# Kernel tuning notes

Measured on AMD Instinct MI355X. Metric: run time of the kernel, lower is better.

## Reference

```python
import jax, jax.numpy as jnp
import numpy as np

B, T, CIN = 8, 4096, 512
GROUP, ENTRY = 2, 320
COUT = 512
D = COUT // GROUP  # per-group codebook dim = 256


def setup_inputs() -> dict:
    key = jax.random.key(0)
    k_x, k_w, k_cb, k_g = jax.random.split(key, 4)
    x = jax.random.normal(k_x, (B, T, CIN), dtype=jnp.float32)
    # weight_proj: Linear(in_channel, group*entry)
    Wp = jax.random.normal(k_w, (GROUP * ENTRY, CIN), dtype=jnp.float32) * (1.0 / np.sqrt(CIN))
    bp = jnp.zeros((GROUP * ENTRY,), dtype=jnp.float32)
    # stacked codebooks: [group, entry, out_channel//group]
    codebooks = jax.random.normal(k_cb, (GROUP, ENTRY, D), dtype=jnp.float32)
    # pre-sampled gumbel noise (torch gumbel_softmax samples this internally)
    gumbel = jax.random.gumbel(k_g, (B, T, GROUP * ENTRY), dtype=jnp.float32)
    return {"x": x, "Wp": Wp, "bp": bp, "codebooks": codebooks, "gumbel": gumbel}


def reference(x, Wp, bp, codebooks, gumbel):
    # weight_proj
    logits = jnp.einsum('btc,ec->bte', x, Wp) + bp          # [B,T,group*entry]
    # gumbel_softmax(tau=1, hard=False, dim=-1): softmax over full group*entry axis
    y = jax.nn.softmax(logits + gumbel, axis=-1)            # [B,T,group*entry]
    # chunk into groups -> contiguous reshape matches torch.chunk
    yg = y.reshape(B, T, GROUP, ENTRY)                      # [B,T,G,E]
    # per-group matmul against codebook weights, then concat over groups
    out = jnp.einsum('btge,ged->btgd', yg, codebooks)       # [B,T,G,D]
    return out.reshape(B, T, GROUP * D)                     # [B,T,out_channel]
```

## Files before the change

kernel.cpp:

```cpp
#include <hip/hip_runtime.h>
#include <hip/hip_bf16.h>
#include <stdint.h>

#define BT     32768
#define CIN    512
#define NE     640
#define ENTRY  320
#define DD     256
#define MROWS  32
#define TPB    256

using bf16x8 = __attribute__((ext_vector_type(8))) short;
using f32x4  = __attribute__((ext_vector_type(4))) float;

#define A_OFF   0
#define A_STR   80
#define B_OFF   2560
#define Y_OFF   0
#define Y_STR   648
#define S_OFF   41472
#define CB_OFF  41600
#define SMEM_BYTES 74368

__device__ __forceinline__ unsigned short f2b(float f) {
    union { float f; uint32_t u; } v; v.f = f;
    uint32_t u = v.u;
    return (unsigned short)((u + 0x7FFFu + ((u >> 16) & 1u)) >> 16);
}

__device__ __forceinline__ void gl2lds16(const void* g, void* l) {
    __builtin_amdgcn_global_load_lds((const __attribute__((address_space(1))) void*)g,
                                     (__attribute__((address_space(3))) void*)l, 16, 0, 0);
}

__global__ void prep_kernel(const float* __restrict__ Wp, const float* __restrict__ cb,
                            unsigned short* __restrict__ WpB, unsigned short* __restrict__ cbT) {
    int i = blockIdx.x * blockDim.x + threadIdx.x;
    if (i < NE * CIN) {
        WpB[i] = f2b(Wp[i]);
    } else {
        int o = i - NE * CIN;
        if (o < 2 * ENTRY * DD) {
            int g = o / (DD * ENTRY);
            int r = o - g * (DD * ENTRY);
            int d = r / ENTRY;
            int e = r - d * ENTRY;
            cbT[o] = f2b(cb[(g * ENTRY + e) * DD + d]);
        }
    }
}

__global__ __launch_bounds__(TPB, 2) void fused_kernel(
    const float* __restrict__ x, const float* __restrict__ bp,
    const float* __restrict__ gum, const unsigned short* __restrict__ WpB,
    const unsigned short* __restrict__ cbT, float* __restrict__ out) {

    extern __shared__ char smem[];
    unsigned short* yS = (unsigned short*)(smem + Y_OFF);
    float*          sS = (float*)(smem + S_OFF);
    char*           aS = smem + A_OFF;
    char*           bS = smem + B_OFF;
    char*           cS = smem + CB_OFF;

    const int tid = threadIdx.x;
    const int w  = tid >> 6;
    const int l  = tid & 63;
    const int q  = l >> 4;
    const int ln = l & 15;
    const int rowbase = blockIdx.x * MROWS;

    f32x4 acc1[2][10];
    const f32x4 fz = {0.f, 0.f, 0.f, 0.f};
#pragma unroll
    for (int rt = 0; rt < 2; ++rt)
#pragma unroll
        for (int ct = 0; ct < 10; ++ct) acc1[rt][ct] = fz;

    const int ar  = tid >> 3;
    const int akq = tid & 7;
    const float* xrow = x + (rowbase + ar) * CIN + akq * 4;

#pragma unroll 1
    for (int ks = 0; ks < 16; ++ks) {
        const int k0 = ks * 32;
        __syncthreads();
        float4 xv = *(const float4*)(xrow + k0);
        ushort4 hv;
        hv.x = f2b(xv.x); hv.y = f2b(xv.y); hv.z = f2b(xv.z); hv.w = f2b(xv.w);
        *(ushort4*)(aS + ar * A_STR + akq * 8) = hv;
#pragma unroll
        for (int i = 0; i < 10; ++i) {
            int cbase = i * 256 + (w << 6);
            int c = cbase + l;
            int e = c >> 2;
            int q2 = (c & 3) ^ ((e >> 1) & 3);
            gl2lds16(WpB + e * CIN + k0 + q2 * 8, bS + cbase * 16);
        }
        __syncthreads();
        bf16x8 af[2];
#pragma unroll
        for (int rt = 0; rt < 2; ++rt)
            af[rt] = *(const bf16x8*)(aS + (rt * 16 + ln) * A_STR + q * 16);
        bf16x8 bfr[10];
#pragma unroll
        for (int ct = 0; ct < 10; ++ct) {
            int e = w * 160 + ct * 16 + ln;
            int ch = e * 4 + (q ^ ((e >> 1) & 3));
            bfr[ct] = *(const bf16x8*)(bS + ch * 16);
        }
#pragma unroll
        for (int rt = 0; rt < 2; ++rt)
#pragma unroll
            for (int ct = 0; ct < 10; ++ct)
                acc1[rt][ct] = __builtin_amdgcn_mfma_f32_16x16x32_bf16(af[rt], bfr[ct], acc1[rt][ct], 0, 0, 0);
    }

    __syncthreads();
    if (tid < MROWS) sS[tid] = 0.0f;
    __syncthreads();

    float bpv[10];
#pragma unroll
    for (int ct = 0; ct < 10; ++ct) bpv[ct] = bp[w * 160 + ct * 16 + ln];

    const float* gbase = gum + (size_t)rowbase * NE + w * 160 + ln;
    float gv[10];
    {
        const float* p0 = gbase + (size_t)(q * 4) * NE;
#pragma unroll
        for (int ct = 0; ct < 10; ++ct) gv[ct] = p0[ct * 16];
    }
#pragma unroll
    for (int ri = 0; ri < 8; ++ri) {
        float gn[10];
        if (ri < 7) {
            int nrow = ((ri + 1) >> 2) * 16 + q * 4 + ((ri + 1) & 3);
            const float* pn = gbase + (size_t)nrow * NE;
#pragma unroll
            for (int ct = 0; ct < 10; ++ct) gn[ct] = pn[ct * 16];
        }
        int rt = ri >> 2, r = ri & 3;
        int row = rt * 16 + q * 4 + r;
        float p = 0.f;
#pragma unroll
        for (int ct = 0; ct < 10; ++ct) {
            int col = w * 160 + ct * 16 + ln;
            float v = acc1[rt][ct][r] + bpv[ct] + gv[ct];
            float e = __expf(v);
            yS[row * Y_STR + col] = f2b(e);
            p += e;
        }
        p += __shfl_xor(p, 1);
        p += __shfl_xor(p, 2);
        p += __shfl_xor(p, 4);
        p += __shfl_xor(p, 8);
        if (ln == 0) atomicAdd(&sS[row], p);
#pragma unroll
        for (int ct = 0; ct < 10; ++ct) gv[ct] = gn[ct];
    }

    f32x4 acc2[2][8];
#pragma unroll
    for (int rt = 0; rt < 2; ++rt)
#pragma unroll
        for (int ct = 0; ct < 8; ++ct) acc2[rt][ct] = fz;

    const int g  = w >> 1;
    const int nb = (w & 1) * 128;

#pragma unroll 1
    for (int ks = 0; ks < 10; ++ks) {
        const int k0 = ks * 32;
        __syncthreads();
#pragma unroll
        for (int i = 0; i < 8; ++i) {
            int cbase = i * 256 + (w << 6);
            int c = cbase + l;
            int gg = c >> 10;
            int cc = c & 1023;
            int n = cc >> 2;
            int q2 = (cc & 3) ^ ((n >> 1) & 3);
            gl2lds16(cbT + (gg * DD + n) * ENTRY + k0 + q2 * 8, cS + cbase * 16);
        }
        __syncthreads();
        bf16x8 af[2];
#pragma unroll
        for (int rt = 0; rt < 2; ++rt)
            af[rt] = *(const bf16x8*)((char*)yS + (rt * 16 + ln) * (Y_STR * 2) + (g * ENTRY + k0 + q * 8) * 2);
        bf16x8 bfr[8];
#pragma unroll
        for (int ct = 0; ct < 8; ++ct) {
            int n = nb + ct * 16 + ln;
            int ch = (g << 10) + n * 4 + (q ^ ((n >> 1) & 3));
            bfr[ct] = *(const bf16x8*)(cS + ch * 16);
        }
#pragma unroll
        for (int rt = 0; rt < 2; ++rt)
#pragma unroll
            for (int ct = 0; ct < 8; ++ct)
                acc2[rt][ct] = __builtin_amdgcn_mfma_f32_16x16x32_bf16(af[rt], bfr[ct], acc2[rt][ct], 0, 0, 0);
    }

#pragma unroll
    for (int rt = 0; rt < 2; ++rt) {
#pragma unroll
        for (int r = 0; r < 4; ++r) {
            int row = rt * 16 + q * 4 + r;
            float inv = 1.0f / sS[row];
            int orow = (rowbase + row) * 512;
#pragma unroll
            for (int ct = 0; ct < 8; ++ct) {
                int col = g * DD + nb + ct * 16 + ln;
                out[orow + col] = acc2[rt][ct][r] * inv;
            }
        }
    }
}

extern "C" void kernel_launch(void* const* d_in, const int* in_sizes, int n_in,
                              void* d_out, int out_size, void* d_ws, size_t ws_size,
                              hipStream_t stream) {
    const float* x   = (const float*)d_in[0];
    const float* Wp  = (const float*)d_in[1];
    const float* bp  = (const float*)d_in[2];
    const float* cb  = (const float*)d_in[3];
    const float* gum = (const float*)d_in[4];
    float* out = (float*)d_out;

    unsigned short* WpB = (unsigned short*)d_ws;
    unsigned short* cbT = WpB + NE * CIN;

    int prep_total = NE * CIN + 2 * ENTRY * DD;
    prep_kernel<<<(prep_total + 255) / 256, 256, 0, stream>>>(Wp, cb, WpB, cbT);

    fused_kernel<<<dim3(BT / MROWS), dim3(TPB), SMEM_BYTES, stream>>>(x, bp, gum, WpB, cbT, out);
}
```

Measured before the change: 251.0 us.

## Double rows per block to reuse projection weights, prefetch x into registers

Raises the block tile from 32 to 64 rows so each staged Wp k-slice feeds four row tiles of MFMAs instead of two, halving weight traffic into LDS per row. The x tile is now loaded one k-step ahead into registers, and the per-step sync pattern is restructured. The softmax and codebook stages run twice over 32-row halves, reusing the same LDS buffer. The cost is more accumulator registers (acc1 grows to 40 vectors), which may reduce occupancy or cause spills, and half as many blocks.

Result: slower. 485.3 us (+93.3%).

```diff
diff --git a/kernel.cpp b/kernel.cpp
--- a/kernel.cpp
+++ b/kernel.cpp
@@ -7,17 +7,19 @@
 #define NE     640
 #define ENTRY  320
 #define DD     256
-#define MROWS  32
+#define MROWS  64
 #define TPB    256
 
 using bf16x8 = __attribute__((ext_vector_type(8))) short;
 using f32x4  = __attribute__((ext_vector_type(4))) float;
+using u16x8  = __attribute__((ext_vector_type(8))) unsigned short;
 
 #define A_OFF   0
 #define A_STR   80
-#define B_OFF   2560
+#define B_OFF   5120
 #define Y_OFF   0
-#define Y_STR   648
+#define Y_STRE  648
+#define Y_STRB  1296
 #define S_OFF   41472
 #define CB_OFF  41600
 #define SMEM_BYTES 74368
@@ -69,25 +71,22 @@
     const int ln = l & 15;
     const int rowbase = blockIdx.x * MROWS;
 
-    f32x4 acc1[2][10];
+    f32x4 acc1[4][10];
     const f32x4 fz = {0.f, 0.f, 0.f, 0.f};
 #pragma unroll
-    for (int rt = 0; rt < 2; ++rt)
+    for (int rt = 0; rt < 4; ++rt)
 #pragma unroll
         for (int ct = 0; ct < 10; ++ct) acc1[rt][ct] = fz;
 
-    const int ar  = tid >> 3;
-    const int akq = tid & 7;
-    const float* xrow = x + (rowbase + ar) * CIN + akq * 4;
+    const int ar  = tid >> 2;
+    const int akq = tid & 3;
+    const float* xrow = x + (size_t)(rowbase + ar) * CIN + akq * 8;
+    float4 xa = *(const float4*)(xrow);
+    float4 xb = *(const float4*)(xrow + 4);
 
 #pragma unroll 1
     for (int ks = 0; ks < 16; ++ks) {
         const int k0 = ks * 32;
-        __syncthreads();
-        float4 xv = *(const float4*)(xrow + k0);
-        ushort4 hv;
-        hv.x = f2b(xv.x); hv.y = f2b(xv.y); hv.z = f2b(xv.z); hv.w = f2b(xv.w);
-        *(ushort4*)(aS + ar * A_STR + akq * 8) = hv;
 #pragma unroll
         for (int i = 0; i < 10; ++i) {
             int cbase = i * 256 + (w << 6);
@@ -96,122 +95,139 @@
             int q2 = (c & 3) ^ ((e >> 1) & 3);
             gl2lds16(WpB + e * CIN + k0 + q2 * 8, bS + cbase * 16);
         }
-        __syncthreads();
-        bf16x8 af[2];
-#pragma unroll
-        for (int rt = 0; rt < 2; ++rt)
+        u16x8 hv;
+        hv[0] = f2b(xa.x); hv[1] = f2b(xa.y); hv[2] = f2b(xa.z); hv[3] = f2b(xa.w);
+        hv[4] = f2b(xb.x); hv[5] = f2b(xb.y); hv[6] = f2b(xb.z); hv[7] = f2b(xb.w);
+        *(u16x8*)(aS + ar * A_STR + akq * 16) = hv;
+        if (ks < 15) {
+            xa = *(const float4*)(xrow + (ks + 1) * 32);
+            xb = *(const float4*)(xrow + (ks + 1) * 32 + 4);
+        }
+        __syncthreads();
+        bf16x8 af[4];
+#pragma unroll
+        for (int rt = 0; rt < 4; ++rt)
             af[rt] = *(const bf16x8*)(aS + (rt * 16 + ln) * A_STR + q * 16);
-        bf16x8 bfr[10];
-#pragma unroll
-        for (int ct = 0; ct < 10; ++ct) {
-            int e = w * 160 + ct * 16 + ln;
-            int ch = e * 4 + (q ^ ((e >> 1) & 3));
-            bfr[ct] = *(const bf16x8*)(bS + ch * 16);
-        }
-#pragma unroll
-        for (int rt = 0; rt < 2; ++rt)
-#pragma unroll
-            for (int ct = 0; ct < 10; ++ct)
-                acc1[rt][ct] = __builtin_amdgcn_mfma_f32_16x16x32_bf16(af[rt], bfr[ct], acc1[rt][ct], 0, 0, 0);
+#pragma unroll
+        for (int g5 = 0; g5 < 2; ++g5) {
+            bf16x8 bfr[5];
+#pragma unroll
+            for (int j = 0; j < 5; ++j) {
+                int e = w * 160 + (g5 * 5 + j) * 16 + ln;
+                int ch = e * 4 + (q ^ ((e >> 1) & 3));
+                bfr[j] = *(const bf16x8*)(bS + ch * 16);
+            }
+#pragma unroll
+            for (int rt = 0; rt < 4; ++rt)
+#pragma unroll
+                for (int j = 0; j < 5; ++j)
+                    acc1[rt][g5 * 5 + j] =
+                        __builtin_amdgcn_mfma_f32_16x16x32_bf16(af[rt], bfr[j], acc1[rt][g5 * 5 + j], 0, 0, 0);
+        }
+        __syncthreads();
     }
 
-    __syncthreads();
-    if (tid < MROWS) sS[tid] = 0.0f;
-    __syncthreads();
-
     float bpv[10];
 #pragma unroll
     for (int ct = 0; ct < 10; ++ct) bpv[ct] = bp[w * 160 + ct * 16 + ln];
-
-    const float* gbase = gum + (size_t)rowbase * NE + w * 160 + ln;
-    float gv[10];
-    {
-        const float* p0 = gbase + (size_t)(q * 4) * NE;
-#pragma unroll
-        for (int ct = 0; ct < 10; ++ct) gv[ct] = p0[ct * 16];
-    }
-#pragma unroll
-    for (int ri = 0; ri < 8; ++ri) {
-        float gn[10];
-        if (ri < 7) {
-            int nrow = ((ri + 1) >> 2) * 16 + q * 4 + ((ri + 1) & 3);
-            const float* pn = gbase + (size_t)nrow * NE;
-#pragma unroll
-            for (int ct = 0; ct < 10; ++ct) gn[ct] = pn[ct * 16];
-        }
-        int rt = ri >> 2, r = ri & 3;
-        int row = rt * 16 + q * 4 + r;
-        float p = 0.f;
-#pragma unroll
-        for (int ct = 0; ct < 10; ++ct) {
-            int col = w * 160 + ct * 16 + ln;
-            float v = acc1[rt][ct][r] + bpv[ct] + gv[ct];
-            float e = __expf(v);
-            yS[row * Y_STR + col] = f2b(e);
-            p += e;
-        }
-        p += __shfl_xor(p, 1);
-        p += __shfl_xor(p, 2);
-        p += __shfl_xor(p, 4);
-        p += __shfl_xor(p, 8);
-        if (ln == 0) atomicAdd(&sS[row], p);
-#pragma unroll
-        for (int ct = 0; ct < 10; ++ct) gv[ct] = gn[ct];
-    }
-
-    f32x4 acc2[2][8];
-#pragma unroll
-    for (int rt = 0; rt < 2; ++rt)
-#pragma unroll
-        for (int ct = 0; ct < 8; ++ct) acc2[rt][ct] = fz;
 
     const int g  = w >> 1;
     const int nb = (w & 1) * 128;
 
 #pragma unroll 1
-    for (int ks = 0; ks < 10; ++ks) {
-        const int k0 = ks * 32;
-        __syncthreads();
-#pragma unroll
-        for (int i = 0; i < 8; ++i) {
-            int cbase = i * 256 + (w << 6);
-            int c = cbase + l;
-            int gg = c >> 10;
-            int cc = c & 1023;
-            int n = cc >> 2;
-            int q2 = (cc & 3) ^ ((n >> 1) & 3);
-            gl2lds16(cbT + (gg * DD + n) * ENTRY + k0 + q2 * 8, cS + cbase * 16);
-        }
-        __syncthreads();
-        bf16x8 af[2];
-#pragma unroll
-        for (int rt = 0; rt < 2; ++rt)
-            af[rt] = *(const bf16x8*)((char*)yS + (rt * 16 + ln) * (Y_STR * 2) + (g * ENTRY + k0 + q * 8) * 2);
-        bf16x8 bfr[8];
-#pragma unroll
-        for (int ct = 0; ct < 8; ++ct) {
-            int n = nb + ct * 16 + ln;
-            int ch = (g << 10) + n * 4 + (q ^ ((n >> 1) & 3));
-            bfr[ct] = *(const bf16x8*)(cS + ch * 16);
-        }
-#pragma unroll
-        for (int rt = 0; rt < 2; ++rt)
-#pragma unroll
-            for (int ct = 0; ct < 8; ++ct)
-                acc2[rt][ct] = __builtin_amdgcn_mfma_f32_16x16x32_bf16(af[rt], bfr[ct], acc2[rt][ct], 0, 0, 0);
-    }
-
-#pragma unroll
-    for (int rt = 0; rt < 2; ++rt) {
-#pragma unroll
-        for (int r = 0; r < 4; ++r) {
-            int row = rt * 16 + q * 4 + r;
-            float inv = 1.0f / sS[row];
-            int orow = (rowbase + row) * 512;
+    for (int h = 0; h < 2; ++h) {
+        __syncthreads();
+        if (tid < 32) sS[tid] = 0.0f;
+        const float* gb = gum + (size_t)(rowbase + 32 * h) * NE + w * 160 + ln;
+        float gv[10];
+        {
+            const float* p0 = gb + (size_t)(q * 4) * NE;
+#pragma unroll
+            for (int ct = 0; ct < 10; ++ct) gv[ct] = p0[ct * 16];
+        }
+        __syncthreads();
+
+#pragma unroll
+        for (int rr = 0; rr < 8; ++rr) {
+            float gn[10];
+            if (rr < 7) {
+                int nrl = ((rr + 1) >> 2) * 16 + q * 4 + ((rr + 1) & 3);
+                const float* pn = gb + (size_t)nrl * NE;
+#pragma unroll
+                for (int ct = 0; ct < 10; ++ct) gn[ct] = pn[ct * 16];
+            }
+            int rt = 2 * h + (rr >> 2);
+            int r  = rr & 3;
+            int row_l = (rr >> 2) * 16 + q * 4 + r;
+            float p = 0.f;
+#pragma unroll
+            for (int ct = 0; ct < 10; ++ct) {
+                int col = w * 160 + ct * 16 + ln;
+                float v = acc1[rt][ct][r] + bpv[ct] + gv[ct];
+                float e = __expf(v);
+                yS[row_l * Y_STRE + col] = f2b(e);
+                p += e;
+            }
+            p += __shfl_xor(p, 1);
+            p += __shfl_xor(p, 2);
+            p += __shfl_xor(p, 4);
+            p += __shfl_xor(p, 8);
+            if (ln == 0) atomicAdd(&sS[row_l], p);
+#pragma unroll
+            for (int ct = 0; ct < 10; ++ct) gv[ct] = gn[ct];
+        }
+
+        f32x4 acc2[2][8];
+#pragma unroll
+        for (int rt2 = 0; rt2 < 2; ++rt2)
+#pragma unroll
+            for (int ct = 0; ct < 8; ++ct) acc2[rt2][ct] = fz;
+
+#pragma unroll 1
+        for (int ks = 0; ks < 10; ++ks) {
+            const int k0 = ks * 32;
+#pragma unroll
+            for (int i = 0; i < 8; ++i) {
+                int cbase = i * 256 + (w << 6);
+                int c = cbase + l;
+                int gg = c >> 10;
+                int cc = c & 1023;
+                int d = cc >> 2;
+                int q2 = (c & 3) ^ ((d >> 1) & 3);
+                gl2lds16(cbT + (gg * DD + d) * ENTRY + k0 + q2 * 8, cS + cbase * 16);
+            }
+            __syncthreads();
+            bf16x8 af2[2];
+#pragma unroll
+            for (int rt2 = 0; rt2 < 2; ++rt2)
+                af2[rt2] = *(const bf16x8*)((char*)yS + (rt2 * 16 + ln) * Y_STRB + (g * ENTRY + k0 + q * 8) * 2);
+            bf16x8 bf2[8];
 #pragma unroll
             for (int ct = 0; ct < 8; ++ct) {
-                int col = g * DD + nb + ct * 16 + ln;
-                out[orow + col] = acc2[rt][ct][r] * inv;
+                int d = nb + ct * 16 + ln;
+                int ch = (g << 10) + d * 4 + (q ^ ((d >> 1) & 3));
+                bf2[ct] = *(const bf16x8*)(cS + ch * 16);
+            }
+#pragma unroll
+            for (int rt2 = 0; rt2 < 2; ++rt2)
+#pragma unroll
+                for (int ct = 0; ct < 8; ++ct)
+                    acc2[rt2][ct] = __builtin_amdgcn_mfma_f32_16x16x32_bf16(af2[rt2], bf2[ct], acc2[rt2][ct], 0, 0, 0);
+            __syncthreads();
+        }
+
+#pragma unroll
+        for (int rt2 = 0; rt2 < 2; ++rt2) {
+#pragma unroll
+            for (int r = 0; r < 4; ++r) {
+                int row_l = rt2 * 16 + q * 4 + r;
+                float inv = 1.0f / sS[row_l];
+                int orow = (rowbase + 32 * h + row_l) * 512;
+#pragma unroll
+                for (int ct = 0; ct < 8; ++ct) {
+                    int col = g * DD + nb + ct * 16 + ln;
+                    out[orow + col] = acc2[rt2][ct][r] * inv;
+                }
             }
         }
     }
```
